# Optimization experiments

Measured on AMD Instinct MI355X. Metric: run time of the kernel, lower is better.

The kernel has to match this reference:

```python
import jax, jax.numpy as jnp
import numpy as np

NB_TASKS = 20
CLASSES_PER_TASK = 100  # uniform cfg.increments -> cache_repeat
TOPK = 2
TEMPERATURE = 5.0  # cfg.task_temperature


def setup_inputs() -> dict:
    key = jax.random.key(0)
    k1, k2, k3 = jax.random.split(key, 3)
    B = 8192
    N = NB_TASKS * CLASSES_PER_TASK
    return {
        "gol": jax.random.normal(k1, (B, NB_TASKS), dtype=jnp.float32),
        "gocls": jax.random.normal(k2, (B, N), dtype=jnp.float32),
        "do_logit": jax.random.normal(k3, (B, N), dtype=jnp.float32),
        "alpha": jnp.array([0.5], dtype=jnp.float32),
    }


def _masked(gol_use, do_logit):
    # mask_ = softmax(gol_use / T, dim=1).repeat_interleave(cache_repeat, dim=1)
    soft = jax.nn.softmax(gol_use / TEMPERATURE, axis=1)  # [B, T]
    # topk hard mask, scattered then repeated; hard*soft repeated == repeat(hard*soft)
    k = min(gol_use.shape[1], TOPK)
    _, tk = jax.lax.top_k(gol_use, k)  # [B, k] int indices
    B = gol_use.shape[0]
    hard = jnp.zeros_like(gol_use).at[jnp.arange(B)[:, None], tk].set(1.0)
    mask = jnp.repeat(hard * soft, CLASSES_PER_TASK, axis=1)  # [B, N]
    return do_logit * mask


def reference(gol, gocls, do_logit, alpha):
    B = gol.shape[0]
    # gocl = opt_by_task(gate_cls_logit, increments, 'amax'): per-task max over class logits
    gocl = gocls.reshape(B, NB_TASKS, CLASSES_PER_TASK).max(axis=-1)  # [B, T]
    logit_mcm = _masked(gol, do_logit)
    logit_gcl = _masked(gocl, do_logit)
    lamb = alpha  # broadcasts over [B, N]
    logit_mix = lamb * logit_mcm + (1.0 - lamb) * logit_gcl
    return logit_mix
```

## Files before the change

### kernel.cpp

```cpp
#include <hip/hip_runtime.h>
#include <hip/hip_bf16.h>
#include <math.h>

#define NB_TASKS 20
#define CLASSES_PER_TASK 100
#define N_COLS (NB_TASKS * CLASSES_PER_TASK)
#define INV_TEMP (1.0f / 5.0f)
#define ROWS_PER_BLOCK 4

__global__ __launch_bounds__(256) void mix_kernel(
    const float* __restrict__ gol,
    const float* __restrict__ gocls,
    const float* __restrict__ dol,
    const float* __restrict__ alpha_p,
    float* __restrict__ out,
    int B)
{
    const int tid  = threadIdx.x;
    const int wave = tid >> 6;
    const int lane = tid & 63;
    const int b    = blockIdx.x * ROWS_PER_BLOCK + wave;
    if (b >= B) return;

    const float* grow = gocls + (size_t)b * N_COLS;

    float cv = -INFINITY;
    #pragma unroll
    for (int t = 0; t < NB_TASKS; ++t) {
        const float* tp = grow + t * CLASSES_PER_TASK;
        float m = tp[lane];
        if (lane < CLASSES_PER_TASK - 64)
            m = fmaxf(m, tp[64 + lane]);
        #pragma unroll
        for (int off = 32; off; off >>= 1)
            m = fmaxf(m, __shfl_xor(m, off));
        if (lane == t) cv = m;
    }

    float gv = (lane < NB_TASKS) ? gol[(size_t)b * NB_TASKS + lane] : -INFINITY;

    const float a = alpha_p[0];

    float wsum = 0.0f;
    #pragma unroll
    for (int path = 0; path < 2; ++path) {
        const float v    = (path == 0) ? gv : cv;
        const float coef = (path == 0) ? a  : (1.0f - a);

        float v1 = v; int j1 = lane;
        #pragma unroll
        for (int off = 32; off; off >>= 1) {
            float ov = __shfl_xor(v1, off);
            int   oj = __shfl_xor(j1, off);
            if (ov > v1 || (ov == v1 && oj < j1)) { v1 = ov; j1 = oj; }
        }

        float ex  = (lane < NB_TASKS) ? __expf((v - v1) * INV_TEMP) : 0.0f;
        float sum = ex;
        #pragma unroll
        for (int off = 32; off; off >>= 1)
            sum += __shfl_xor(sum, off);

        float v2 = (lane == j1) ? -INFINITY : v;
        int   j2 = lane;
        #pragma unroll
        for (int off = 32; off; off >>= 1) {
            float ov = __shfl_xor(v2, off);
            int   oj = __shfl_xor(j2, off);
            if (ov > v2 || (ov == v2 && oj < j2)) { v2 = ov; j2 = oj; }
        }

        if (lane == j1 || lane == j2)
            wsum += coef * ex * (1.0f / sum);
    }

    const float4* din  = (const float4*)(dol + (size_t)b * N_COLS);
    float4*       dout = (float4*)(out + (size_t)b * N_COLS);

    #pragma unroll
    for (int i = 0; i < (N_COLS / 4 + 63) / 64; ++i) {
        const int f = lane + 64 * i;
        if (f < N_COLS / 4) {
            const float wgt = __shfl(wsum, f / (CLASSES_PER_TASK / 4));
            float4 r;
            if (wgt != 0.0f) {
                float4 v = din[f];
                r.x = v.x * wgt; r.y = v.y * wgt; r.z = v.z * wgt; r.w = v.w * wgt;
            } else {
                r.x = r.y = r.z = r.w = 0.0f;
            }
            dout[f] = r;
        }
    }
}

extern "C" void kernel_launch(void* const* d_in, const int* in_sizes, int n_in,
                              void* d_out, int out_size, void* d_ws, size_t ws_size,
                              hipStream_t stream) {
    const float* gol   = (const float*)d_in[0];
    const float* gocls = (const float*)d_in[1];
    const float* dol   = (const float*)d_in[2];
    const float* alpha = (const float*)d_in[3];
    float* out = (float*)d_out;

    const int B = in_sizes[0] / NB_TASKS;

    const int grid = (B + ROWS_PER_BLOCK - 1) / ROWS_PER_BLOCK;
    hipLaunchKernelGGL(mix_kernel, dim3(grid), dim3(256), 0, stream,
                       gol, gocls, dol, alpha, out, B);
}
```

Before: 31.18 us.

## Vectorize per-task max loads and broadcast top-2 weights as scalars

Each wave now reads the class logits as float4, with four 16-lane groups each handling one task at a time. This replaces twenty scalar passes with five vector passes and shortens the max reductions. The top-2/softmax selection is rewritten to reduce over 32 lanes and broadcast the two indices and weights through readfirstlane. The output loop then picks each task's weight with scalar compares instead of a per-element shuffle. The goal is to cut load-instruction count and cross-lane shuffle overhead; the kernel stays bound by memory bandwidth.

```diff
diff --git a/kernel.cpp b/kernel.cpp
--- a/kernel.cpp
+++ b/kernel.cpp
@@ -8,6 +8,44 @@
 #define INV_TEMP (1.0f / 5.0f)
 #define ROWS_PER_BLOCK 4
 
+__device__ __forceinline__ float rfl_f(float x) {
+    return __int_as_float(__builtin_amdgcn_readfirstlane(__float_as_int(x)));
+}
+
+struct Top2 { int j1, j2; float w1, w2; };
+
+__device__ __forceinline__ Top2 softmax_top2(float v, float coef, int lane) {
+    float v1 = v; int i1 = lane;
+    #pragma unroll
+    for (int off = 16; off; off >>= 1) {
+        float ov = __shfl_xor(v1, off);
+        int   oj = __shfl_xor(i1, off);
+        if (ov > v1 || (ov == v1 && oj < i1)) { v1 = ov; i1 = oj; }
+    }
+    float v2 = (lane == i1) ? -INFINITY : v;
+    int   i2 = lane;
+    #pragma unroll
+    for (int off = 16; off; off >>= 1) {
+        float ov = __shfl_xor(v2, off);
+        int   oj = __shfl_xor(i2, off);
+        if (ov > v2 || (ov == v2 && oj < i2)) { v2 = ov; i2 = oj; }
+    }
+    float ex  = __expf((v - v1) * INV_TEMP);
+    float sum = ex;
+    #pragma unroll
+    for (int off = 16; off; off >>= 1)
+        sum += __shfl_xor(sum, off);
+
+    Top2 r;
+    r.j1 = __builtin_amdgcn_readfirstlane(i1);
+    r.j2 = __builtin_amdgcn_readfirstlane(i2);
+    float w1 = coef / sum;
+    float w2 = __expf((v2 - v1) * INV_TEMP) * w1;
+    r.w1 = rfl_f(w1);
+    r.w2 = rfl_f(w2);
+    return r;
+}
+
 __global__ __launch_bounds__(256) void mix_kernel(
     const float* __restrict__ gol,
     const float* __restrict__ gocls,
@@ -17,62 +55,37 @@
     int B)
 {
     const int tid  = threadIdx.x;
-    const int wave = tid >> 6;
     const int lane = tid & 63;
-    const int b    = blockIdx.x * ROWS_PER_BLOCK + wave;
+    const int b    = blockIdx.x * ROWS_PER_BLOCK + (tid >> 6);
     if (b >= B) return;
+
+    const int grp = lane >> 4;
+    const int s   = lane & 15;
 
     const float* grow = gocls + (size_t)b * N_COLS;
 
+    const float a  = alpha_p[0];
+    const float gv = (lane < NB_TASKS) ? gol[(size_t)b * NB_TASKS + lane] : -INFINITY;
+
     float cv = -INFINITY;
     #pragma unroll
-    for (int t = 0; t < NB_TASKS; ++t) {
-        const float* tp = grow + t * CLASSES_PER_TASK;
-        float m = tp[lane];
-        if (lane < CLASSES_PER_TASK - 64)
-            m = fmaxf(m, tp[64 + lane]);
+    for (int k = 0; k < 5; ++k) {
+        const float4* p = (const float4*)(grow + (4 * k + grp) * CLASSES_PER_TASK);
+        float4 v0 = p[s];
+        float m = fmaxf(fmaxf(v0.x, v0.y), fmaxf(v0.z, v0.w));
+        if (s < 25 - 16) {
+            float4 v1 = p[16 + s];
+            m = fmaxf(m, fmaxf(fmaxf(v1.x, v1.y), fmaxf(v1.z, v1.w)));
+        }
         #pragma unroll
-        for (int off = 32; off; off >>= 1)
+        for (int off = 8; off; off >>= 1)
             m = fmaxf(m, __shfl_xor(m, off));
-        if (lane == t) cv = m;
+        float g2 = __shfl(m, (lane & 3) << 4);
+        if ((lane >> 2) == k) cv = g2;
     }
 
-    float gv = (lane < NB_TASKS) ? gol[(size_t)b * NB_TASKS + lane] : -INFINITY;
-
-    const float a = alpha_p[0];
-
-    float wsum = 0.0f;
-    #pragma unroll
-    for (int path = 0; path < 2; ++path) {
-        const float v    = (path == 0) ? gv : cv;
-        const float coef = (path == 0) ? a  : (1.0f - a);
-
-        float v1 = v; int j1 = lane;
-        #pragma unroll
-        for (int off = 32; off; off >>= 1) {
-            float ov = __shfl_xor(v1, off);
-            int   oj = __shfl_xor(j1, off);
-            if (ov > v1 || (ov == v1 && oj < j1)) { v1 = ov; j1 = oj; }
-        }
-
-        float ex  = (lane < NB_TASKS) ? __expf((v - v1) * INV_TEMP) : 0.0f;
-        float sum = ex;
-        #pragma unroll
-        for (int off = 32; off; off >>= 1)
-            sum += __shfl_xor(sum, off);
-
-        float v2 = (lane == j1) ? -INFINITY : v;
-        int   j2 = lane;
-        #pragma unroll
-        for (int off = 32; off; off >>= 1) {
-            float ov = __shfl_xor(v2, off);
-            int   oj = __shfl_xor(j2, off);
-            if (ov > v2 || (ov == v2 && oj < j2)) { v2 = ov; j2 = oj; }
-        }
-
-        if (lane == j1 || lane == j2)
-            wsum += coef * ex * (1.0f / sum);
-    }
+    const Top2 pa = softmax_top2(gv, a,        lane);
+    const Top2 pb = softmax_top2(cv, 1.0f - a, lane);
 
     const float4* din  = (const float4*)(dol + (size_t)b * N_COLS);
     float4*       dout = (float4*)(out + (size_t)b * N_COLS);
@@ -81,7 +94,12 @@
     for (int i = 0; i < (N_COLS / 4 + 63) / 64; ++i) {
         const int f = lane + 64 * i;
         if (f < N_COLS / 4) {
-            const float wgt = __shfl(wsum, f / (CLASSES_PER_TASK / 4));
+            const int task = f / (CLASSES_PER_TASK / 4);
+            float wgt = 0.0f;
+            wgt += (task == pa.j1) ? pa.w1 : 0.0f;
+            wgt += (task == pa.j2) ? pa.w2 : 0.0f;
+            wgt += (task == pb.j1) ? pb.w1 : 0.0f;
+            wgt += (task == pb.j2) ? pb.w2 : 0.0f;
             float4 r;
             if (wgt != 0.0f) {
                 float4 v = din[f];
```

New measurement: 28.18 us. 9.6% less time.
